# Kernel tuning notes

Measured on AMD Instinct MI355X. Metric: run time of the kernel, lower is better.

## Reference

```python
import jax, jax.numpy as jnp
import numpy as np

N_NODES = 10000
N_EDGES = 640000
IN_DIM, HID_DIM, OUT_DIM = 128, 512, 512


def setup_inputs() -> dict:
    key = jax.random.key(0)
    k1, k2, k3, k4, k5, k6 = jax.random.split(key, 6)
    feat = jax.random.normal(k1, (N_NODES, IN_DIM), dtype=jnp.float32)
    edge_index = jax.random.randint(k2, (2, N_EDGES), 0, N_NODES, dtype=jnp.int64)
    s1 = 1.0 / np.sqrt(IN_DIM)
    s2 = 1.0 / np.sqrt(HID_DIM)
    W1 = jax.random.uniform(k3, (IN_DIM, HID_DIM), jnp.float32, -s1, s1)
    b1 = jnp.zeros((HID_DIM,), jnp.float32)
    W2 = jax.random.uniform(k4, (HID_DIM, OUT_DIM), jnp.float32, -s2, s2)
    b2 = jnp.zeros((OUT_DIM,), jnp.float32)
    return {"feat": feat, "edge_index": edge_index, "W1": W1, "b1": b1, "W2": W2, "b2": b2}


def _degree_norms(edge_index, n_nodes):
    src, dst = edge_index[0], edge_index[1]
    ones = jnp.ones((edge_index.shape[1],), jnp.float32)
    out_deg = jax.ops.segment_sum(ones, src, num_segments=n_nodes)
    in_deg = jax.ops.segment_sum(ones, dst, num_segments=n_nodes)
    # DGL clamps degree to >= 1 to avoid division by zero
    norm_src = jax.lax.rsqrt(jnp.maximum(out_deg, 1.0))  # [N]
    norm_dst = jax.lax.rsqrt(jnp.maximum(in_deg, 1.0))   # [N]
    return norm_src, norm_dst


def _graph_conv(x, src, dst, norm_src, norm_dst, W, b, n_nodes):
    # norm='both': D_in^{-1/2} A D_out^{-1/2} X W + b
    x = x * norm_src[:, None]
    agg = jax.ops.segment_sum(x[src], dst, num_segments=n_nodes)  # [N, d]
    agg = agg * norm_dst[:, None]
    return agg @ W + b


def reference(feat, edge_index, W1, b1, W2, b2):
    n = feat.shape[0]
    src, dst = edge_index[0], edge_index[1]
    norm_src, norm_dst = _degree_norms(edge_index, n)
    h = _graph_conv(feat, src, dst, norm_src, norm_dst, W1, b1, n)
    h = jax.nn.relu(h)
    out = _graph_conv(h, src, dst, norm_src, norm_dst, W2, b2, n)
    return out
```

## Files before the change

### kernel.cpp

```cpp
#include <hip/hip_runtime.h>

#define NN 10000
#define NE 640000
#define IN_DIM 128
#define HID_DIM 512
#define OUT_DIM 512
#define NB 10240
#define P_PART 128
#define EPB (NE / P_PART)

typedef __attribute__((ext_vector_type(8))) short short8;
typedef __attribute__((ext_vector_type(4))) float f32x4;
typedef __attribute__((ext_vector_type(2))) float f32x2;

__device__ __forceinline__ ushort f2b(float f) {
    union { float f; uint i; } c; c.f = f;
    uint x = c.i;
    uint r = (x + 0x7fffu + ((x >> 16) & 1u)) >> 16;
    return (ushort)r;
}
__device__ __forceinline__ float blo(uint a) {
    union { uint i; float f; } c; c.i = a << 16; return c.f;
}
__device__ __forceinline__ float bhi(uint a) {
    union { uint i; float f; } c; c.i = a & 0xffff0000u; return c.f;
}

__global__ __launch_bounds__(1024) void hist_kernel(const int* __restrict__ ei,
                                                    ushort* __restrict__ pcnt_dst,
                                                    ushort* __restrict__ pcnt_src) {
    __shared__ int h[NB];
    int p = blockIdx.x;
    const int* __restrict__ idx = (blockIdx.y == 0) ? (ei + NE) : ei;
    ushort* __restrict__ outp = (blockIdx.y == 0) ? pcnt_dst : pcnt_src;
    int t = threadIdx.x;
    for (int i = t; i < NB; i += 1024) h[i] = 0;
    __syncthreads();
    int base = p * EPB;
    for (int i = t; i < EPB; i += 1024) atomicAdd(&h[idx[base + i]], 1);
    __syncthreads();
    for (int i = t; i < NB; i += 1024) outp[p * NB + i] = (ushort)h[i];
}

__global__ __launch_bounds__(256) void colreduce_kernel(const ushort* __restrict__ pcnt_dst,
                                                        const ushort* __restrict__ pcnt_src,
                                                        int* __restrict__ poff,
                                                        int* __restrict__ deg_in,
                                                        float* __restrict__ norm_src,
                                                        float* __restrict__ norm_dst) {
    int v = blockIdx.x * 256 + threadIdx.x;
    int s = 0;
#pragma unroll 4
    for (int p = 0; p < P_PART; p++) {
        int c = pcnt_dst[p * NB + v];
        poff[p * NB + v] = s;
        s += c;
    }
    deg_in[v] = s;
    int s2 = 0;
#pragma unroll 4
    for (int p = 0; p < P_PART; p++) s2 += pcnt_src[p * NB + v];
    if (v < NN) {
        norm_dst[v] = rsqrtf(fmaxf((float)s, 1.0f));
        norm_src[v] = rsqrtf(fmaxf((float)s2, 1.0f));
    }
}

__global__ __launch_bounds__(1024) void scan_kernel(const int* __restrict__ deg,
                                                    int* __restrict__ row_off) {
    const int PER = NB / 1024;
    __shared__ int lds[1024];
    int t = threadIdx.x;
    int base = t * PER;
    int local[PER];
    int s = 0;
#pragma unroll
    for (int i = 0; i < PER; i++) {
        int v = deg[base + i];
        local[i] = s;
        s += v;
    }
    lds[t] = s;
    __syncthreads();
    for (int off = 1; off < 1024; off <<= 1) {
        int x = (t >= off) ? lds[t - off] : 0;
        __syncthreads();
        lds[t] += x;
        __syncthreads();
    }
    int excl = lds[t] - s;
#pragma unroll
    for (int i = 0; i < PER; i++) {
        int idx = base + i;
        if (idx <= NN) row_off[idx] = excl + local[i];
    }
}

__global__ __launch_bounds__(1024) void fill_kernel(const int* __restrict__ src,
                                                    const int* __restrict__ dst,
                                                    const int* __restrict__ row_off,
                                                    const int* __restrict__ poff,
                                                    int* __restrict__ csr_src) {
    __shared__ int cur[NB];
    int p = blockIdx.x, t = threadIdx.x;
    for (int i = t; i < NB; i += 1024)
        cur[i] = ((i < NN) ? row_off[i] : 0) + poff[p * NB + i];
    __syncthreads();
    int base = p * EPB;
    for (int i = t; i < EPB; i += 1024) {
        int d = dst[base + i];
        int slot = atomicAdd(&cur[d], 1);
        csr_src[slot] = src[base + i];
    }
}

__global__ __launch_bounds__(256) void densep_kernel(const float* __restrict__ feat,
                                                     const float* __restrict__ norm_src,
                                                     ushort* __restrict__ featb,
                                                     const float* __restrict__ W1,
                                                     ushort* __restrict__ W1t,
                                                     const float* __restrict__ W2,
                                                     ushort* __restrict__ W2t) {
    __shared__ float tld[32][33];
    int b = blockIdx.x;
    if (b < 1250) {
        int i = b * 256 + threadIdx.x;
        if (i < NN * IN_DIM / 4) {
            float4 v = ((const float4*)feat)[i];
            float s = norm_src[i >> 5];
            ushort4 o;
            o.x = f2b(v.x * s); o.y = f2b(v.y * s); o.z = f2b(v.z * s); o.w = f2b(v.w * s);
            ((ushort4*)featb)[i] = o;
        }
        return;
    }
    const float* W; ushort* Wt; int K, N, k0, n0;
    if (b < 1250 + 64) {
        int bb = b - 1250;
        W = W1; Wt = W1t; K = IN_DIM; N = HID_DIM;
        k0 = (bb & 3) * 32; n0 = (bb >> 2) * 32;
    } else {
        int bb = b - 1250 - 64;
        W = W2; Wt = W2t; K = HID_DIM; N = OUT_DIM;
        k0 = (bb & 15) * 32; n0 = (bb >> 4) * 32;
    }
    int tx = threadIdx.x & 31, ty = threadIdx.x >> 5;
#pragma unroll
    for (int r = 0; r < 32; r += 8)
        tld[ty + r][tx] = W[(size_t)(k0 + ty + r) * N + n0 + tx];
    __syncthreads();
#pragma unroll
    for (int r = 0; r < 32; r += 8)
        Wt[(size_t)(n0 + ty + r) * K + k0 + tx] = f2b(tld[tx][ty + r]);
}

__global__ __launch_bounds__(64) void agg1_kernel(const uint* __restrict__ fb,
                                                  const int* __restrict__ row_off,
                                                  const int* __restrict__ csr_src,
                                                  const float* __restrict__ norm_dst,
                                                  uint* __restrict__ aggb) {
    int node = blockIdx.x;
    uint lane = threadIdx.x;
    int beg = row_off[node], end = row_off[node + 1];
    f32x2 acc = {0.f, 0.f};
    int i = beg;
    for (; i + 7 < end; i += 8) {
        uint u[8]; uint a[8];
#pragma unroll
        for (int j = 0; j < 8; j++) u[j] = (uint)csr_src[i + j];
#pragma unroll
        for (int j = 0; j < 8; j++) a[j] = fb[u[j] * 64u + lane];
#pragma unroll
        for (int j = 0; j < 8; j++) {
            f32x2 v; v.x = blo(a[j]); v.y = bhi(a[j]);
            acc += v;
        }
    }
    for (; i < end; i++) {
        uint a = fb[(uint)csr_src[i] * 64u + lane];
        f32x2 v; v.x = blo(a); v.y = bhi(a);
        acc += v;
    }
    float nd = norm_dst[node];
    aggb[node * 64 + lane] = (uint)f2b(acc.x * nd) | ((uint)f2b(acc.y * nd) << 16);
}

__global__ __launch_bounds__(64) void agg2_kernel(const uint* __restrict__ hb,
                                                  const int* __restrict__ row_off,
                                                  const int* __restrict__ csr_src,
                                                  const float* __restrict__ norm_dst,
                                                  uint* __restrict__ aggb) {
    int node = blockIdx.x;
    uint t = blockIdx.y * 64 + threadIdx.x;
    int beg = row_off[node], end = row_off[node + 1];
    f32x2 acc = {0.f, 0.f};
    int i = beg;
    for (; i + 7 < end; i += 8) {
        uint u[8]; uint a[8];
#pragma unroll
        for (int j = 0; j < 8; j++) u[j] = (uint)csr_src[i + j];
#pragma unroll
        for (int j = 0; j < 8; j++) a[j] = hb[u[j] * 256u + t];
#pragma unroll
        for (int j = 0; j < 8; j++) {
            f32x2 v; v.x = blo(a[j]); v.y = bhi(a[j]);
            acc += v;
        }
    }
    for (; i < end; i++) {
        uint a = hb[(uint)csr_src[i] * 256u + t];
        f32x2 v; v.x = blo(a); v.y = bhi(a);
        acc += v;
    }
    float nd = norm_dst[node];
    aggb[node * 256 + t] = (uint)f2b(acc.x * nd) | ((uint)f2b(acc.y * nd) << 16);
}

template <int EPI>
__global__ __launch_bounds__(256) void gemm_bf16_kernel(const ushort* __restrict__ A,
                                                        const ushort* __restrict__ Bt,
                                                        const float* __restrict__ bias,
                                                        const float* __restrict__ scale,
                                                        void* __restrict__ Cout,
                                                        int M, int K, int N) {
    const int BM = 128;
    __shared__ __align__(16) ushort As[BM * 32];
    __shared__ __align__(16) ushort Bs[64 * 32];
    int tid = threadIdx.x;
    int lane = tid & 63;
    int wid = tid >> 6;
    int bm = blockIdx.x * BM;
    int bn = blockIdx.y * 64;
    int wm = (wid & 1) * 64;
    int wn = (wid >> 1) * 32;

    f32x4 acc[4][2] = {};

    for (int k0 = 0; k0 < K; k0 += 32) {
        __syncthreads();
#pragma unroll
        for (int u = 0; u < 2; u++) {
            int l = u * 256 + tid;
            int row = l >> 2, kq = l & 3;
            int gm = bm + row;
            uint4 v = make_uint4(0u, 0u, 0u, 0u);
            if (gm < M) v = *(const uint4*)(A + (size_t)gm * K + k0 + kq * 8);
            int j = ((row >> 4) << 6) + (kq << 4) + (row & 15);
            *(uint4*)(As + j * 8) = v;
        }
        {
            int row = tid >> 2, kq = tid & 3;
            uint4 v = *(const uint4*)(Bt + (size_t)(bn + row) * K + k0 + kq * 8);
            int j = ((row >> 4) << 6) + (kq << 4) + (row & 15);
            *(uint4*)(Bs + j * 8) = v;
        }
        __syncthreads();
        short8 af[4], bfr[2];
#pragma unroll
        for (int i = 0; i < 4; i++) {
            int j = (((wm >> 4) + i) << 6) + ((lane >> 4) << 4) + (lane & 15);
            af[i] = *(const short8*)(As + j * 8);
        }
#pragma unroll
        for (int i = 0; i < 2; i++) {
            int j = (((wn >> 4) + i) << 6) + ((lane >> 4) << 4) + (lane & 15);
            bfr[i] = *(const short8*)(Bs + j * 8);
        }
#pragma unroll
        for (int i = 0; i < 4; i++)
#pragma unroll
            for (int jn = 0; jn < 2; jn++)
                acc[i][jn] = __builtin_amdgcn_mfma_f32_16x16x32_bf16(af[i], bfr[jn], acc[i][jn], 0, 0, 0);
    }

#pragma unroll
    for (int i = 0; i < 4; i++) {
#pragma unroll
        for (int jn = 0; jn < 2; jn++) {
            int col = bn + wn + jn * 16 + (lane & 15);
            float bv = bias[col];
#pragma unroll
            for (int r = 0; r < 4; r++) {
                int gm = bm + wm + i * 16 + ((lane >> 4) << 2) + r;
                if (gm < M) {
                    float v = acc[i][jn][r] + bv;
                    if (EPI == 1) {
                        v = fmaxf(v, 0.f) * scale[gm];
                        ((ushort*)Cout)[(size_t)gm * N + col] = f2b(v);
                    } else {
                        ((float*)Cout)[(size_t)gm * N + col] = v;
                    }
                }
            }
        }
    }
}

extern "C" void kernel_launch(void* const* d_in, const int* in_sizes, int n_in,
                              void* d_out, int out_size, void* d_ws, size_t ws_size,
                              hipStream_t stream) {
    const float* feat = (const float*)d_in[0];
    const int* ei = (const int*)d_in[1];
    const float* W1 = (const float*)d_in[2];
    const float* b1 = (const float*)d_in[3];
    const float* W2 = (const float*)d_in[4];
    const float* b2 = (const float*)d_in[5];
    float* out = (float*)d_out;

    const int* src = ei;
    const int* dst = ei + NE;

    char* ws = (char*)d_ws;
    size_t off = 0;
    auto alloc = [&](size_t bytes) -> void* {
        void* p = ws + off;
        off += (bytes + 255) & ~(size_t)255;
        return p;
    };
    int* row_off = (int*)alloc((NN + 16) * sizeof(int));
    int* deg_in = (int*)alloc(NB * sizeof(int));
    float* norm_src = (float*)alloc(NN * sizeof(float));
    float* norm_dst = (float*)alloc(NN * sizeof(float));
    int* csr_src = (int*)alloc(NE * sizeof(int));
    ushort* featb = (ushort*)alloc((size_t)NN * IN_DIM * 2);
    ushort* W1t = (ushort*)alloc((size_t)HID_DIM * IN_DIM * 2);
    ushort* W2t = (ushort*)alloc((size_t)OUT_DIM * HID_DIM * 2);
    size_t union_base = off;
    ushort* pcnt_dst = (ushort*)alloc((size_t)P_PART * NB * sizeof(ushort));
    ushort* pcnt_src = (ushort*)alloc((size_t)P_PART * NB * sizeof(ushort));
    int* poff = (int*)alloc((size_t)P_PART * NB * sizeof(int));
    off = union_base;
    ushort* agg1b = (ushort*)alloc((size_t)NN * IN_DIM * 2);
    ushort* hb = (ushort*)alloc((size_t)NN * HID_DIM * 2);
    ushort* agg2b = (ushort*)alloc((size_t)NN * HID_DIM * 2);

    {
        dim3 g(P_PART, 2);
        hist_kernel<<<g, 1024, 0, stream>>>(ei, pcnt_dst, pcnt_src);
    }
    colreduce_kernel<<<NB / 256, 256, 0, stream>>>(pcnt_dst, pcnt_src, poff, deg_in, norm_src, norm_dst);
    scan_kernel<<<1, 1024, 0, stream>>>(deg_in, row_off);
    fill_kernel<<<P_PART, 1024, 0, stream>>>(src, dst, row_off, poff, csr_src);

    densep_kernel<<<1250 + 64 + 256, 256, 0, stream>>>(feat, norm_src, featb, W1, W1t, W2, W2t);

    agg1_kernel<<<NN, 64, 0, stream>>>((const uint*)featb, row_off, csr_src, norm_dst, (uint*)agg1b);
    {
        dim3 grid((NN + 127) / 128, HID_DIM / 64);
        gemm_bf16_kernel<1><<<grid, 256, 0, stream>>>(agg1b, W1t, b1, norm_src, hb, NN, IN_DIM, HID_DIM);
    }
    {
        dim3 grid(NN, 4);
        agg2_kernel<<<grid, 64, 0, stream>>>((const uint*)hb, row_off, csr_src, norm_dst, (uint*)agg2b);
    }
    {
        dim3 grid((NN + 127) / 128, OUT_DIM / 64);
        gemm_bf16_kernel<0><<<grid, 256, 0, stream>>>(agg2b, W2t, b2, nullptr, out, NN, HID_DIM, OUT_DIM);
    }
}
```

Baseline: 137.8 us.

## Fuse prep kernels, use direct global-to-LDS loads in GEMM, scalarize gather indices

Merges the weight transpose into the histogram kernel and the feature scaling into the scan kernel, which removes the separate dense-prep launch. In the GEMM, the per-thread staging of A and B tiles into LDS is replaced by global_load_lds 16-byte direct loads. To allow this, the out-of-range row guard is dropped and the aggregate buffers are padded to 10112 rows. The aggregation kernels read neighbour indices through readfirstlane so row addresses become scalar. Risks: the padded rows are read uninitialised and only masked at store, and the direct LDS loads depend on the per-wave layout matching the previous swizzle.

Measured after the change: 136.3 us. Within noise of the previous version (-1.1%).

```diff
diff --git a/kernel.cpp b/kernel.cpp
--- a/kernel.cpp
+++ b/kernel.cpp
@@ -26,20 +26,48 @@
     union { uint i; float f; } c; c.i = a & 0xffff0000u; return c.f;
 }
 
-__global__ __launch_bounds__(1024) void hist_kernel(const int* __restrict__ ei,
-                                                    ushort* __restrict__ pcnt_dst,
-                                                    ushort* __restrict__ pcnt_src) {
+__device__ __forceinline__ void gl_lds16(const ushort* g, ushort* l) {
+    __builtin_amdgcn_global_load_lds((const __attribute__((address_space(1))) uint*)g,
+                                     (__attribute__((address_space(3))) uint*)l, 16, 0, 0);
+}
+
+__global__ __launch_bounds__(1024) void histw_kernel(const int* __restrict__ ei,
+                                                     ushort* __restrict__ pcnt_dst,
+                                                     ushort* __restrict__ pcnt_src,
+                                                     const float* __restrict__ W1,
+                                                     ushort* __restrict__ W1t,
+                                                     const float* __restrict__ W2,
+                                                     ushort* __restrict__ W2t) {
     __shared__ int h[NB];
-    int p = blockIdx.x;
-    const int* __restrict__ idx = (blockIdx.y == 0) ? (ei + NE) : ei;
-    ushort* __restrict__ outp = (blockIdx.y == 0) ? pcnt_dst : pcnt_src;
+    int b = blockIdx.x;
     int t = threadIdx.x;
-    for (int i = t; i < NB; i += 1024) h[i] = 0;
+    if (b < 256) {
+        int p = b & 127;
+        const int* __restrict__ idx = (b < 128) ? (ei + NE) : ei;
+        ushort* __restrict__ outp = (b < 128) ? pcnt_dst : pcnt_src;
+        for (int i = t; i < NB; i += 1024) h[i] = 0;
+        __syncthreads();
+        int base = p * EPB;
+        for (int i = t; i < EPB; i += 1024) atomicAdd(&h[idx[base + i]], 1);
+        __syncthreads();
+        for (int i = t; i < NB; i += 1024) outp[p * NB + i] = (ushort)h[i];
+        return;
+    }
+    float* tld = (float*)h;
+    const float* W; ushort* Wt; int K, N, k0, n0;
+    if (b < 320) {
+        int bb = b - 256;
+        W = W1; Wt = W1t; K = IN_DIM; N = HID_DIM;
+        k0 = (bb & 3) * 32; n0 = (bb >> 2) * 32;
+    } else {
+        int bb = b - 320;
+        W = W2; Wt = W2t; K = HID_DIM; N = OUT_DIM;
+        k0 = (bb & 15) * 32; n0 = (bb >> 4) * 32;
+    }
+    int r = t >> 5, c = t & 31;
+    tld[r * 33 + c] = W[(size_t)(k0 + r) * N + n0 + c];
     __syncthreads();
-    int base = p * EPB;
-    for (int i = t; i < EPB; i += 1024) atomicAdd(&h[idx[base + i]], 1);
-    __syncthreads();
-    for (int i = t; i < NB; i += 1024) outp[p * NB + i] = (ushort)h[i];
+    Wt[(size_t)(n0 + r) * K + k0 + c] = f2b(tld[c * 33 + r]);
 }
 
 __global__ __launch_bounds__(256) void colreduce_kernel(const ushort* __restrict__ pcnt_dst,
@@ -66,33 +94,48 @@
     }
 }
 
-__global__ __launch_bounds__(1024) void scan_kernel(const int* __restrict__ deg,
-                                                    int* __restrict__ row_off) {
-    const int PER = NB / 1024;
-    __shared__ int lds[1024];
+__global__ __launch_bounds__(1024) void scanfeat_kernel(const int* __restrict__ deg,
+                                                        int* __restrict__ row_off,
+                                                        const float* __restrict__ feat,
+                                                        const float* __restrict__ norm_src,
+                                                        ushort* __restrict__ featb) {
+    int b = blockIdx.x;
     int t = threadIdx.x;
-    int base = t * PER;
-    int local[PER];
-    int s = 0;
-#pragma unroll
-    for (int i = 0; i < PER; i++) {
-        int v = deg[base + i];
-        local[i] = s;
-        s += v;
-    }
-    lds[t] = s;
-    __syncthreads();
-    for (int off = 1; off < 1024; off <<= 1) {
-        int x = (t >= off) ? lds[t - off] : 0;
-        __syncthreads();
-        lds[t] += x;
-        __syncthreads();
-    }
-    int excl = lds[t] - s;
-#pragma unroll
-    for (int i = 0; i < PER; i++) {
-        int idx = base + i;
-        if (idx <= NN) row_off[idx] = excl + local[i];
+    if (b == 0) {
+        const int PER = NB / 1024;
+        __shared__ int lds[1024];
+        int base = t * PER;
+        int local[PER];
+        int s = 0;
+#pragma unroll
+        for (int i = 0; i < PER; i++) {
+            int v = deg[base + i];
+            local[i] = s;
+            s += v;
+        }
+        lds[t] = s;
+        __syncthreads();
+        for (int off = 1; off < 1024; off <<= 1) {
+            int x = (t >= off) ? lds[t - off] : 0;
+            __syncthreads();
+            lds[t] += x;
+            __syncthreads();
+        }
+        int excl = lds[t] - s;
+#pragma unroll
+        for (int i = 0; i < PER; i++) {
+            int idx = base + i;
+            if (idx <= NN) row_off[idx] = excl + local[i];
+        }
+        return;
+    }
+    int i = (b - 1) * 1024 + t;
+    if (i < NN * IN_DIM / 4) {
+        float4 v = ((const float4*)feat)[i];
+        float s = norm_src[i >> 5];
+        ushort4 o;
+        o.x = f2b(v.x * s); o.y = f2b(v.y * s); o.z = f2b(v.z * s); o.w = f2b(v.w * s);
+        ((ushort4*)featb)[i] = o;
     }
 }
 
@@ -114,46 +157,6 @@
     }
 }
 
-__global__ __launch_bounds__(256) void densep_kernel(const float* __restrict__ feat,
-                                                     const float* __restrict__ norm_src,
-                                                     ushort* __restrict__ featb,
-                                                     const float* __restrict__ W1,
-                                                     ushort* __restrict__ W1t,
-                                                     const float* __restrict__ W2,
-                                                     ushort* __restrict__ W2t) {
-    __shared__ float tld[32][33];
-    int b = blockIdx.x;
-    if (b < 1250) {
-        int i = b * 256 + threadIdx.x;
-        if (i < NN * IN_DIM / 4) {
-            float4 v = ((const float4*)feat)[i];
-            float s = norm_src[i >> 5];
-            ushort4 o;
-            o.x = f2b(v.x * s); o.y = f2b(v.y * s); o.z = f2b(v.z * s); o.w = f2b(v.w * s);
-            ((ushort4*)featb)[i] = o;
-        }
-        return;
-    }
-    const float* W; ushort* Wt; int K, N, k0, n0;
-    if (b < 1250 + 64) {
-        int bb = b - 1250;
-        W = W1; Wt = W1t; K = IN_DIM; N = HID_DIM;
-        k0 = (bb & 3) * 32; n0 = (bb >> 2) * 32;
-    } else {
-        int bb = b - 1250 - 64;
-        W = W2; Wt = W2t; K = HID_DIM; N = OUT_DIM;
-        k0 = (bb & 15) * 32; n0 = (bb >> 4) * 32;
-    }
-    int tx = threadIdx.x & 31, ty = threadIdx.x >> 5;
-#pragma unroll
-    for (int r = 0; r < 32; r += 8)
-        tld[ty + r][tx] = W[(size_t)(k0 + ty + r) * N + n0 + tx];
-    __syncthreads();
-#pragma unroll
-    for (int r = 0; r < 32; r += 8)
-        Wt[(size_t)(n0 + ty + r) * K + k0 + tx] = f2b(tld[tx][ty + r]);
-}
-
 __global__ __launch_bounds__(64) void agg1_kernel(const uint* __restrict__ fb,
                                                   const int* __restrict__ row_off,
                                                   const int* __restrict__ csr_src,
@@ -164,12 +167,14 @@
     int beg = row_off[node], end = row_off[node + 1];
     f32x2 acc = {0.f, 0.f};
     int i = beg;
-    for (; i + 7 < end; i += 8) {
-        uint u[8]; uint a[8];
-#pragma unroll
-        for (int j = 0; j < 8; j++) u[j] = (uint)csr_src[i + j];
-#pragma unroll
-        for (int j = 0; j < 8; j++) a[j] = fb[u[j] * 64u + lane];
+    for (; i + 8 <= end; i += 8) {
+        const uint* rp[8];
+#pragma unroll
+        for (int j = 0; j < 8; j++)
+            rp[j] = fb + (uint)__builtin_amdgcn_readfirstlane(csr_src[i + j]) * 64u;
+        uint a[8];
+#pragma unroll
+        for (int j = 0; j < 8; j++) a[j] = rp[j][lane];
 #pragma unroll
         for (int j = 0; j < 8; j++) {
             f32x2 v; v.x = blo(a[j]); v.y = bhi(a[j]);
@@ -177,7 +182,8 @@
         }
     }
     for (; i < end; i++) {
-        uint a = fb[(uint)csr_src[i] * 64u + lane];
+        const uint* rp = fb + (uint)__builtin_amdgcn_readfirstlane(csr_src[i]) * 64u;
+        uint a = rp[lane];
         f32x2 v; v.x = blo(a); v.y = bhi(a);
         acc += v;
     }
@@ -195,12 +201,14 @@
     int beg = row_off[node], end = row_off[node + 1];
     f32x2 acc = {0.f, 0.f};
     int i = beg;
-    for (; i + 7 < end; i += 8) {
-        uint u[8]; uint a[8];
-#pragma unroll
-        for (int j = 0; j < 8; j++) u[j] = (uint)csr_src[i + j];
-#pragma unroll
-        for (int j = 0; j < 8; j++) a[j] = hb[u[j] * 256u + t];
+    for (; i + 8 <= end; i += 8) {
+        const uint* rp[8];
+#pragma unroll
+        for (int j = 0; j < 8; j++)
+            rp[j] = hb + (uint)__builtin_amdgcn_readfirstlane(csr_src[i + j]) * 256u;
+        uint a[8];
+#pragma unroll
+        for (int j = 0; j < 8; j++) a[j] = rp[j][t];
 #pragma unroll
         for (int j = 0; j < 8; j++) {
             f32x2 v; v.x = blo(a[j]); v.y = bhi(a[j]);
@@ -208,7 +216,8 @@
         }
     }
     for (; i < end; i++) {
-        uint a = hb[(uint)csr_src[i] * 256u + t];
+        const uint* rp = hb + (uint)__builtin_amdgcn_readfirstlane(csr_src[i]) * 256u;
+        uint a = rp[t];
         f32x2 v; v.x = blo(a); v.y = bhi(a);
         acc += v;
     }
@@ -234,26 +243,24 @@
     int wm = (wid & 1) * 64;
     int wn = (wid >> 1) * 32;
 
+    int cA0 = tid, cA1 = 256 + tid, cB = tid;
+    int rowA0 = ((cA0 >> 6) << 4) | (cA0 & 15), kqA0 = (cA0 >> 4) & 3;
+    int rowA1 = ((cA1 >> 6) << 4) | (cA1 & 15), kqA1 = (cA1 >> 4) & 3;
+    int rowB = ((cB >> 6) << 4) | (cB & 15), kqB = (cB >> 4) & 3;
+    const ushort* srcA0 = A + (size_t)(bm + rowA0) * K + kqA0 * 8;
+    const ushort* srcA1 = A + (size_t)(bm + rowA1) * K + kqA1 * 8;
+    const ushort* srcB = Bt + (size_t)(bn + rowB) * K + kqB * 8;
+    ushort* ldsA0 = As + (wid * 64) * 8;
+    ushort* ldsA1 = As + (256 + wid * 64) * 8;
+    ushort* ldsB = Bs + (wid * 64) * 8;
+
     f32x4 acc[4][2] = {};
 
     for (int k0 = 0; k0 < K; k0 += 32) {
         __syncthreads();
-#pragma unroll
-        for (int u = 0; u < 2; u++) {
-            int l = u * 256 + tid;
-            int row = l >> 2, kq = l & 3;
-            int gm = bm + row;
-            uint4 v = make_uint4(0u, 0u, 0u, 0u);
-            if (gm < M) v = *(const uint4*)(A + (size_t)gm * K + k0 + kq * 8);
-            int j = ((row >> 4) << 6) + (kq << 4) + (row & 15);
-            *(uint4*)(As + j * 8) = v;
-        }
-        {
-            int row = tid >> 2, kq = tid & 3;
-            uint4 v = *(const uint4*)(Bt + (size_t)(bn + row) * K + k0 + kq * 8);
-            int j = ((row >> 4) << 6) + (kq << 4) + (row & 15);
-            *(uint4*)(Bs + j * 8) = v;
-        }
+        gl_lds16(srcA0 + k0, ldsA0);
+        gl_lds16(srcA1 + k0, ldsA1);
+        gl_lds16(srcB + k0, ldsB);
         __syncthreads();
         short8 af[4], bfr[2];
 #pragma unroll
@@ -309,6 +316,7 @@
 
     const int* src = ei;
     const int* dst = ei + NE;
+    const int NNP = 10112;
 
     char* ws = (char*)d_ws;
     size_t off = 0;
@@ -330,23 +338,18 @@
     ushort* pcnt_src = (ushort*)alloc((size_t)P_PART * NB * sizeof(ushort));
     int* poff = (int*)alloc((size_t)P_PART * NB * sizeof(int));
     off = union_base;
-    ushort* agg1b = (ushort*)alloc((size_t)NN * IN_DIM * 2);
+    ushort* agg1b = (ushort*)alloc((size_t)NNP * IN_DIM * 2);
     ushort* hb = (ushort*)alloc((size_t)NN * HID_DIM * 2);
-    ushort* agg2b = (ushort*)alloc((size_t)NN * HID_DIM * 2);
-
-    {
-        dim3 g(P_PART, 2);
-        hist_kernel<<<g, 1024, 0, stream>>>(ei, pcnt_dst, pcnt_src);
-    }
+    ushort* agg2b = (ushort*)alloc((size_t)NNP * HID_DIM * 2);
+
+    histw_kernel<<<576, 1024, 0, stream>>>(ei, pcnt_dst, pcnt_src, W1, W1t, W2, W2t);
     colreduce_kernel<<<NB / 256, 256, 0, stream>>>(pcnt_dst, pcnt_src, poff, deg_in, norm_src, norm_dst);
-    scan_kernel<<<1, 1024, 0, stream>>>(deg_in, row_off);
+    scanfeat_kernel<<<314, 1024, 0, stream>>>(deg_in, row_off, feat, norm_src, featb);
     fill_kernel<<<P_PART, 1024, 0, stream>>>(src, dst, row_off, poff, csr_src);
-
-    densep_kernel<<<1250 + 64 + 256, 256, 0, stream>>>(feat, norm_src, featb, W1, W1t, W2, W2t);
 
     agg1_kernel<<<NN, 64, 0, stream>>>((const uint*)featb, row_off, csr_src, norm_dst, (uint*)agg1b);
     {
-        dim3 grid((NN + 127) / 128, HID_DIM / 64);
+        dim3 grid(NNP / 128, HID_DIM / 64);
         gemm_bf16_kernel<1><<<grid, 256, 0, stream>>>(agg1b, W1t, b1, norm_src, hb, NN, IN_DIM, HID_DIM);
     }
     {
@@ -354,7 +357,7 @@
         agg2_kernel<<<grid, 64, 0, stream>>>((const uint*)hb, row_off, csr_src, norm_dst, (uint*)agg2b);
     }
     {
-        dim3 grid((NN + 127) / 128, OUT_DIM / 64);
+        dim3 grid(NNP / 128, OUT_DIM / 64);
         gemm_bf16_kernel<0><<<grid, 256, 0, stream>>>(agg2b, W2t, b2, nullptr, out, NN, HID_DIM, OUT_DIM);
     }
 }
```
